# Optimization experiments

Hardware: AMD Instinct MI355X
Metric: run time of the kernel (lower is better)

## Reference

```python
import jax, jax.numpy as jnp
import numpy as np

H, W = 200, 200           # BEV spatial shape (single level)
NBQ, NH, NL, NP = 2, 8, 1, 4
D = 256
HD = D // NH


def setup_inputs() -> dict:
    key = jax.random.key(0)
    ks = jax.random.split(key, 12)
    bs, nq = 1, H * W
    query = jax.random.normal(ks[0], (bs, nq, D), jnp.float32)
    value = jax.random.normal(ks[1], (bs, NBQ * nq, D), jnp.float32)
    reference_points = jax.random.uniform(ks[2], (bs, nq, NL, 2), dtype=jnp.float32)
    spatial_shapes = jnp.array([[H, W]], dtype=jnp.int32)
    sc = 1.0 / np.sqrt(D)
    W_v = jax.random.normal(ks[3], (D, D), jnp.float32) * sc
    b_v = jax.random.normal(ks[4], (D,), jnp.float32) * 0.01
    W_so = jax.random.normal(ks[5], (2 * D, NBQ * NH * NL * NP * 2), jnp.float32) * 0.02
    b_so = jax.random.normal(ks[6], (NBQ * NH * NL * NP * 2,), jnp.float32) * 0.5
    W_aw = jax.random.normal(ks[7], (2 * D, NBQ * NH * NL * NP), jnp.float32) * 0.02
    b_aw = jax.random.normal(ks[8], (NBQ * NH * NL * NP,), jnp.float32) * 0.01
    W_o = jax.random.normal(ks[9], (D, D), jnp.float32) * sc
    b_o = jax.random.normal(ks[10], (D,), jnp.float32) * 0.01
    return {"query": query, "value": value, "reference_points": reference_points,
            "spatial_shapes": spatial_shapes,
            "W_v": W_v, "b_v": b_v, "W_so": W_so, "b_so": b_so,
            "W_aw": W_aw, "b_aw": b_aw, "W_o": W_o, "b_o": b_o}


def _ms_deform_attn(value, locs, attn):
    # value: (B, K, NH, HD); locs: (B, nq, NH, NL, NP, 2) in [0,1]; attn: (B, nq, NH, NL, NP)
    B, K, h, d = value.shape
    nq = locs.shape[1]
    out = jnp.zeros((B, nq, h, d), value.dtype)
    start = 0
    for l, (Hl, Wl) in enumerate([(H, W)]):
        v = value[:, start:start + Hl * Wl].transpose(0, 2, 1, 3).reshape(B * h, Hl * Wl, d)
        start += Hl * Wl
        g = locs[:, :, :, l]                      # (B, nq, h, NP, 2)
        # grid_sample(align_corners=False, padding='zeros') pixel coords
        x = g[..., 0] * Wl - 0.5
        y = g[..., 1] * Hl - 0.5
        x0 = jnp.floor(x); y0 = jnp.floor(y)
        lx = x - x0; ly = y - y0
        x0 = x0.astype(jnp.int32); y0 = y0.astype(jnp.int32)
        acc = jnp.zeros((B * h, nq * NP, d), value.dtype)
        for dy, wy in ((0, 1.0 - ly), (1, ly)):
            for dx, wx in ((0, 1.0 - lx), (1, lx)):
                xi = x0 + dx; yi = y0 + dy
                valid = ((xi >= 0) & (xi < Wl) & (yi >= 0) & (yi < Hl)).astype(value.dtype)
                idx = jnp.clip(yi, 0, Hl - 1) * Wl + jnp.clip(xi, 0, Wl - 1)  # (B,nq,h,NP)
                idxf = idx.transpose(0, 2, 1, 3).reshape(B * h, nq * NP)
                samp = jnp.take_along_axis(v, idxf[:, :, None], axis=1)       # (B*h, nq*NP, d)
                wgt = (wx * wy * valid).transpose(0, 2, 1, 3).reshape(B * h, nq * NP, 1)
                acc = acc + samp * wgt
        acc = acc.reshape(B, h, nq, NP, d)
        out = out + jnp.einsum('bhqpd,bqhp->bqhd', acc, attn[:, :, :, l])
    return out.reshape(B, nq, h * d)


def reference(query, value, reference_points, spatial_shapes,
              W_v, b_v, W_so, b_so, W_aw, b_aw, W_o, b_o):
    bs, nq, _ = query.shape
    identity = query
    val4 = value.reshape(bs, NBQ, nq, D)
    # query enhanced with most recent bev-queue features
    qe = jnp.concatenate([val4[:, 0], query], axis=-1)           # (bs, nq, 2D)
    vproj = (value @ W_v + b_v).reshape(bs * NBQ, nq, NH, HD)
    off = (qe @ W_so + b_so).reshape(bs, nq, NH, NBQ, NL, NP, 2)
    aw = (qe @ W_aw + b_aw).reshape(bs, nq, NH, NBQ, NL * NP)
    aw = jax.nn.softmax(aw, axis=-1).reshape(bs, nq, NH, NBQ, NL, NP)
    aw = aw.transpose(0, 3, 1, 2, 4, 5).reshape(bs * NBQ, nq, NH, NL, NP)
    # offset normalizer: [W, H] per level
    norm = jnp.stack([spatial_shapes[:, 1], spatial_shapes[:, 0]], -1).astype(query.dtype)  # (NL,2)
    locs = (reference_points[:, :, None, None, :, None, :]
            + off / norm[None, None, None, None, :, None, :])     # (bs,nq,NH,NBQ,NL,NP,2)
    locs = locs.transpose(0, 3, 1, 2, 4, 5, 6).reshape(bs * NBQ, nq, NH, NL, NP, 2)
    out = _ms_deform_attn(vproj, locs, aw)                        # (bs*NBQ, nq, D)
    out = out.reshape(bs, NBQ, nq, D).mean(axis=1)
    return out @ W_o + b_o + identity
```

## Files before the change

### kernel.cpp

```cpp
#include <hip/hip_runtime.h>
#include <math.h>

#define HW_   40000
#define NQ_   40000
#define IMGW  200
#define IMGH  200

typedef __bf16 bf16;
typedef __attribute__((ext_vector_type(4))) __bf16 bf16x4;
typedef __attribute__((ext_vector_type(8))) __bf16 bf16x8;
typedef __attribute__((ext_vector_type(4))) float f32x4;

__device__ __forceinline__ void gload_lds16(const void* g, void* l) {
  __builtin_amdgcn_global_load_lds(
      (const __attribute__((address_space(1))) void*)g,
      (__attribute__((address_space(3))) void*)l, 16, 0, 0);
}

__global__ __launch_bounds__(256) void prep_kernel(
    const float* __restrict__ Wv, const float* __restrict__ Wso,
    const float* __restrict__ Waw, const float* __restrict__ Wo,
    bf16* __restrict__ BtV, bf16* __restrict__ BtOA, bf16* __restrict__ BtO)
{
  int idx = blockIdx.x * 256 + threadIdx.x;
  if (idx < 65536) {
    int k = idx >> 8, n = idx & 255;
    BtV[(size_t)n * 256 + k] = (bf16)Wv[idx];
  } else if (idx < 131072) {
    int j = idx - 65536;
    int k = j >> 7, n = j & 127;
    BtOA[(size_t)n * 512 + k] = (bf16)Wso[j];
  } else if (idx < 163840) {
    int j = idx - 131072;
    int k = j >> 6, n = j & 63;
    BtOA[(size_t)(128 + n) * 512 + k] = (bf16)Waw[j];
  } else if (idx < 229376) {
    int j = idx - 163840;
    int k = j >> 8, n = j & 255;
    BtO[(size_t)n * 256 + k] = (bf16)Wo[j];
  }
}

template<int KT, int MODE, int BN, int ASRC>
__global__ __launch_bounds__(256) void mfma_gemm_kernel(
    const void* __restrict__ A0, const void* __restrict__ A1,
    const bf16* __restrict__ Bt,
    const float* __restrict__ bias0, const float* __restrict__ bias1,
    const float* __restrict__ resid,
    void* __restrict__ outp, void* __restrict__ outp2, int M)
{
  constexpr int NT16 = BN / 32;
  constexpr int BCH  = BN / 64;
  constexpr int NIT  = KT / 32;
  __shared__ bf16 As[2][64 * 32];
  __shared__ bf16 Bs[2][BN * 32];
  const int t    = threadIdx.x;
  const int m0   = blockIdx.x * 64;
  const int w    = t >> 6;
  const int lane = t & 63;
  const int quad = lane >> 4;
  const int l16  = lane & 15;
  const int wm   = (w & 1) * 32;
  const int wn   = (w >> 1) * (BN / 2);

  f32x4 acc[2][NT16] = {};

  int gmA;
  {
    int gm = m0 + (t >> 2);
    gmA = (gm >= M) ? (M - 1) : gm;
  }
  const int arow = t >> 2;
  const int akey = (arow >> 1) & 3;

  float4 apf[2];
  bf16x8 ah0, ah1;

  auto issueB = [&](int it) {
    const int kt  = it * 32;
    const int buf = it & 1;
#pragma unroll
    for (int i = 0; i < BCH; ++i) {
      int c   = i * 256 + t;
      int row = c >> 2;
      int j   = (c & 3) ^ ((row >> 1) & 3);
      gload_lds16(&Bt[(size_t)row * KT + kt + j * 8], &Bs[buf][c * 8]);
    }
  };

  auto issueA_lds = [&](int it) {
    const int kt  = it * 32;
    const int buf = it & 1;
    const bf16* Ap = (const bf16*)A0;
    int j = (t & 3) ^ akey;
    gload_lds16(&Ap[(size_t)gmA * 256 + kt + j * 8], &As[buf][t * 8]);
  };

  auto loadA_reg = [&](int it) {
    const int kt = it * 32;
    if (ASRC == 1) {
      const float* Ap; int col;
      if (KT == 512) { Ap = (kt < 256) ? (const float*)A0 : (const float*)A1; col = kt & 255; }
      else           { Ap = (const float*)A0; col = kt; }
      const float4* s4 = (const float4*)&Ap[(size_t)gmA * 256 + col + (t & 3) * 8];
      apf[0] = s4[0];
      apf[1] = s4[1];
    } else {
      ah0 = *(const bf16x8*)&((const bf16*)A0)[(size_t)gmA * 256 + kt + (t & 3) * 8];
      ah1 = *(const bf16x8*)&((const bf16*)A1)[(size_t)gmA * 256 + kt + (t & 3) * 8];
    }
  };

  auto writeA = [&](int it) {
    const int buf = it & 1;
    int j = (t & 3) ^ akey;
    bf16x8 o;
    if (ASRC == 1) {
      o = bf16x8{(bf16)apf[0].x, (bf16)apf[0].y, (bf16)apf[0].z, (bf16)apf[0].w,
                 (bf16)apf[1].x, (bf16)apf[1].y, (bf16)apf[1].z, (bf16)apf[1].w};
    } else {
#pragma unroll
      for (int e = 0; e < 8; ++e)
        o[e] = (bf16)(0.5f * ((float)ah0[e] + (float)ah1[e]));
    }
    *(bf16x8*)&As[buf][arow * 32 + j * 8] = o;
  };

  if (ASRC) { loadA_reg(0); issueB(0); writeA(0); }
  else      { issueA_lds(0); issueB(0); }

#pragma unroll
  for (int it = 0; it < NIT; ++it) {
    __syncthreads();
    if (it + 1 < NIT) {
      issueB(it + 1);
      if (ASRC) loadA_reg(it + 1); else issueA_lds(it + 1);
    }
    const bf16* as = As[it & 1];
    const bf16* bs = Bs[it & 1];
    bf16x8 af[2], bfr[NT16];
#pragma unroll
    for (int x = 0; x < 2; ++x) {
      int row = wm + x * 16 + l16;
      af[x] = *(const bf16x8*)&as[row * 32 + (quad ^ ((row >> 1) & 3)) * 8];
    }
#pragma unroll
    for (int x = 0; x < NT16; ++x) {
      int row = wn + x * 16 + l16;
      bfr[x] = *(const bf16x8*)&bs[row * 32 + (quad ^ ((row >> 1) & 3)) * 8];
    }
#pragma unroll
    for (int mt = 0; mt < 2; ++mt)
#pragma unroll
      for (int nt = 0; nt < NT16; ++nt)
        acc[mt][nt] = __builtin_amdgcn_mfma_f32_16x16x32_bf16(
            af[mt], bfr[nt], acc[mt][nt], 0, 0, 0);
    if (ASRC && it + 1 < NIT) writeA(it + 1);
  }

#pragma unroll
  for (int mt = 0; mt < 2; ++mt) {
#pragma unroll
    for (int r = 0; r < 4; ++r) {
      const int gm = m0 + wm + mt * 16 + quad * 4 + r;
      if (gm >= M) continue;
#pragma unroll
      for (int nt = 0; nt < NT16; ++nt) {
        const int gn = wn + nt * 16 + l16;
        float v = acc[mt][nt][r];
        if (MODE == 0) {
          int nbq = (gm >= HW_) ? 1 : 0;
          int pix = gm - nbq * HW_;
          int h = gn >> 5, hd = gn & 31;
          ((bf16*)outp)[(((size_t)(nbq * 8 + h) * HW_ + pix) << 5) + hd] =
              (bf16)(v + bias0[gn]);
        } else if (MODE == 1) {
          if (gn < 128) {
            int gg = gn >> 3, e = gn & 7;
            ((bf16*)outp)[((size_t)gg * NQ_ + gm) * 8 + e] = (bf16)(v + bias0[gn]);
          } else {
            int j = gn - 128;
            int gg = j >> 2, e = j & 3;
            ((bf16*)outp2)[((size_t)gg * NQ_ + gm) * 4 + e] = (bf16)(v + bias1[j]);
          }
        } else {
          ((float*)outp)[(size_t)gm * 256 + gn] =
              v + bias0[gn] + resid[(size_t)gm * 256 + gn];
        }
      }
    }
  }
}

__global__ __launch_bounds__(256) void deform_attn_kernel(
    const bf16* __restrict__ vws,
    const bf16* __restrict__ off_g,
    const bf16* __restrict__ aw_g,
    const float* __restrict__ ref,
    bf16* __restrict__ ms0,
    bf16* __restrict__ ms1)
{
  const int t    = threadIdx.x;
  const int w    = t >> 6;
  const int lane = t & 63;
  const int b    = blockIdx.x;
  const int nbq  = b / 5000;
  const int bb   = b - nbq * 5000;
  const int h    = bb & 7;
  const int qc   = bb >> 3;
  const int qi   = lane >> 2;
  const int sub  = lane & 3;
  const int q    = qc * 64 + w * 16 + qi;
  const int g    = h * 2 + nbq;
  bf16* msN = nbq ? ms1 : ms0;

  const float rx = ref[2 * q + 0] * (float)IMGW - 0.5f;
  const float ry = ref[2 * q + 1] * (float)IMGH - 0.5f;

  bf16x4 a4 = *(const bf16x4*)&aw_g[((size_t)g * NQ_ + q) * 4];
  float aa0 = (float)a4[0], aa1 = (float)a4[1], aa2 = (float)a4[2], aa3 = (float)a4[3];
  float mx = fmaxf(fmaxf(aa0, aa1), fmaxf(aa2, aa3));
  float e0 = __expf(aa0 - mx), e1 = __expf(aa1 - mx);
  float e2 = __expf(aa2 - mx), e3 = __expf(aa3 - mx);
  float inv = 1.0f / (e0 + e1 + e2 + e3);
  float w4[4] = {e0 * inv, e1 * inv, e2 * inv, e3 * inv};

  bf16x8 o8 = *(const bf16x8*)&off_g[((size_t)g * NQ_ + q) * 8];

  const bf16* vbase = vws + (((size_t)(nbq * 8 + h) * HW_) << 5) + sub * 8;

  float  ww[16];
  bf16x8 v[16];
#pragma unroll
  for (int p = 0; p < 4; ++p) {
    float x = rx + (float)o8[2 * p];
    float y = ry + (float)o8[2 * p + 1];
    float xf = floorf(x), yf = floorf(y);
    int   x0 = (int)xf,   y0 = (int)yf;
    float lx = x - xf,    ly = y - yf;
    int   x1 = x0 + 1,    y1 = y0 + 1;
    float w00 = (1.0f - lx) * (1.0f - ly);
    float w01 = lx * (1.0f - ly);
    float w10 = (1.0f - lx) * ly;
    float w11 = lx * ly;
    if (x0 < 0 || x0 >= IMGW) { w00 = 0.0f; w10 = 0.0f; }
    if (x1 < 0 || x1 >= IMGW) { w01 = 0.0f; w11 = 0.0f; }
    if (y0 < 0 || y0 >= IMGH) { w00 = 0.0f; w01 = 0.0f; }
    if (y1 < 0 || y1 >= IMGH) { w10 = 0.0f; w11 = 0.0f; }
    int xc0 = min(max(x0, 0), IMGW - 1), xc1 = min(max(x1, 0), IMGW - 1);
    int yc0 = min(max(y0, 0), IMGH - 1), yc1 = min(max(y1, 0), IMGH - 1);
    float wp = w4[p];
    ww[4 * p + 0] = wp * w00;
    ww[4 * p + 1] = wp * w01;
    ww[4 * p + 2] = wp * w10;
    ww[4 * p + 3] = wp * w11;
    v[4 * p + 0] = *(const bf16x8*)&vbase[(size_t)(yc0 * IMGW + xc0) << 5];
    v[4 * p + 1] = *(const bf16x8*)&vbase[(size_t)(yc0 * IMGW + xc1) << 5];
    v[4 * p + 2] = *(const bf16x8*)&vbase[(size_t)(yc1 * IMGW + xc0) << 5];
    v[4 * p + 3] = *(const bf16x8*)&vbase[(size_t)(yc1 * IMGW + xc1) << 5];
  }

  float acc[8] = {};
#pragma unroll
  for (int s = 0; s < 16; ++s)
#pragma unroll
    for (int j = 0; j < 8; ++j)
      acc[j] = fmaf(ww[s], (float)v[s][j], acc[j]);

  bf16x8 o;
#pragma unroll
  for (int j = 0; j < 8; ++j) o[j] = (bf16)acc[j];
  *(bf16x8*)&msN[(size_t)q * 256 + h * 32 + sub * 8] = o;
}

extern "C" void kernel_launch(void* const* d_in, const int* in_sizes, int n_in,
                              void* d_out, int out_size, void* d_ws, size_t ws_size,
                              hipStream_t stream) {
  const float* query = (const float*)d_in[0];
  const float* value = (const float*)d_in[1];
  const float* ref   = (const float*)d_in[2];
  const float* Wv  = (const float*)d_in[4];
  const float* bv  = (const float*)d_in[5];
  const float* Wso = (const float*)d_in[6];
  const float* bso = (const float*)d_in[7];
  const float* Waw = (const float*)d_in[8];
  const float* baw = (const float*)d_in[9];
  const float* Wo  = (const float*)d_in[10];
  const float* bo  = (const float*)d_in[11];
  float* out = (float*)d_out;

  char* p = (char*)d_ws;
  bf16* vws    = (bf16*)p; p += (size_t)2 * 8 * HW_ * 32 * 2;
  bf16* off_g  = (bf16*)p; p += (size_t)16 * NQ_ * 8 * 2;
  bf16* aw_g   = (bf16*)p; p += (size_t)16 * NQ_ * 4 * 2;
  bf16* ms0    = (bf16*)p; p += (size_t)NQ_ * 256 * 2;
  bf16* ms1    = (bf16*)p; p += (size_t)NQ_ * 256 * 2;
  bf16* BtV    = (bf16*)p; p += (size_t)256 * 256 * 2;
  bf16* BtOA   = (bf16*)p; p += (size_t)192 * 512 * 2;
  bf16* BtO    = (bf16*)p; p += (size_t)256 * 256 * 2;

  prep_kernel<<<896, 256, 0, stream>>>(Wv, Wso, Waw, Wo, BtV, BtOA, BtO);

  mfma_gemm_kernel<256, 0, 256, 1><<<1250, 256, 0, stream>>>(
      value, nullptr, BtV, bv, nullptr, nullptr, vws, nullptr, 2 * HW_);
  mfma_gemm_kernel<512, 1, 192, 1><<<625, 256, 0, stream>>>(
      value, query, BtOA, bso, baw, nullptr, off_g, aw_g, NQ_);
  deform_attn_kernel<<<10000, 256, 0, stream>>>(vws, off_g, aw_g, ref, ms0, ms1);
  mfma_gemm_kernel<256, 2, 256, 2><<<625, 256, 0, stream>>>(
      ms0, ms1, BtO, bo, nullptr, query, out, nullptr, NQ_);
}
```

Measured before the change: 296.3 us.

## Load GEMM fragments directly from global memory, dropping LDS staging

The MFMA GEMM kernel no longer stages A and B tiles through double-buffered shared memory with swizzling and barriers. Each lane now loads its own MFMA fragments straight from global memory into registers, prefetching the next A fragment while the current MFMAs run, and launch bounds now request at least two blocks per CU. This removes the __syncthreads and LDS traffic, but each wave re-reads B and A fragments that other waves share, so it leans on L1/L2 hits, and B loads are no longer prefetched ahead of use.

New measurement: 385.4 us. 1.3x slower.

```diff
diff --git a/kernel.cpp b/kernel.cpp
--- a/kernel.cpp
+++ b/kernel.cpp
@@ -10,12 +10,6 @@
 typedef __attribute__((ext_vector_type(4))) __bf16 bf16x4;
 typedef __attribute__((ext_vector_type(8))) __bf16 bf16x8;
 typedef __attribute__((ext_vector_type(4))) float f32x4;
-
-__device__ __forceinline__ void gload_lds16(const void* g, void* l) {
-  __builtin_amdgcn_global_load_lds(
-      (const __attribute__((address_space(1))) void*)g,
-      (__attribute__((address_space(3))) void*)l, 16, 0, 0);
-}
 
 __global__ __launch_bounds__(256) void prep_kernel(
     const float* __restrict__ Wv, const float* __restrict__ Wso,
@@ -42,7 +36,7 @@
 }
 
 template<int KT, int MODE, int BN, int ASRC>
-__global__ __launch_bounds__(256) void mfma_gemm_kernel(
+__global__ __launch_bounds__(256, 2) void mfma_gemm_kernel(
     const void* __restrict__ A0, const void* __restrict__ A1,
     const bf16* __restrict__ Bt,
     const float* __restrict__ bias0, const float* __restrict__ bias1,
@@ -50,10 +44,7 @@
     void* __restrict__ outp, void* __restrict__ outp2, int M)
 {
   constexpr int NT16 = BN / 32;
-  constexpr int BCH  = BN / 64;
   constexpr int NIT  = KT / 32;
-  __shared__ bf16 As[2][64 * 32];
-  __shared__ bf16 Bs[2][BN * 32];
   const int t    = threadIdx.x;
   const int m0   = blockIdx.x * 64;
   const int w    = t >> 6;
@@ -65,97 +56,75 @@
 
   f32x4 acc[2][NT16] = {};
 
-  int gmA;
-  {
-    int gm = m0 + (t >> 2);
-    gmA = (gm >= M) ? (M - 1) : gm;
-  }
-  const int arow = t >> 2;
-  const int akey = (arow >> 1) & 3;
-
-  float4 apf[2];
-  bf16x8 ah0, ah1;
-
-  auto issueB = [&](int it) {
-    const int kt  = it * 32;
-    const int buf = it & 1;
-#pragma unroll
-    for (int i = 0; i < BCH; ++i) {
-      int c   = i * 256 + t;
-      int row = c >> 2;
-      int j   = (c & 3) ^ ((row >> 1) & 3);
-      gload_lds16(&Bt[(size_t)row * KT + kt + j * 8], &Bs[buf][c * 8]);
-    }
-  };
-
-  auto issueA_lds = [&](int it) {
-    const int kt  = it * 32;
-    const int buf = it & 1;
-    const bf16* Ap = (const bf16*)A0;
-    int j = (t & 3) ^ akey;
-    gload_lds16(&Ap[(size_t)gmA * 256 + kt + j * 8], &As[buf][t * 8]);
-  };
-
-  auto loadA_reg = [&](int it) {
+  int aoff[2];
+#pragma unroll
+  for (int x = 0; x < 2; ++x) {
+    int r = m0 + wm + x * 16 + l16;
+    if (r >= M) r = M - 1;
+    aoff[x] = r * 256 + quad * 8;
+  }
+  int boff[NT16];
+#pragma unroll
+  for (int x = 0; x < NT16; ++x)
+    boff[x] = (wn + x * 16 + l16) * KT + quad * 8;
+
+  float4 apf[2][2];
+  bf16x8 ah[2][2];
+
+  auto loadA = [&](int it) {
     const int kt = it * 32;
     if (ASRC == 1) {
       const float* Ap; int col;
       if (KT == 512) { Ap = (kt < 256) ? (const float*)A0 : (const float*)A1; col = kt & 255; }
       else           { Ap = (const float*)A0; col = kt; }
-      const float4* s4 = (const float4*)&Ap[(size_t)gmA * 256 + col + (t & 3) * 8];
-      apf[0] = s4[0];
-      apf[1] = s4[1];
+#pragma unroll
+      for (int x = 0; x < 2; ++x) {
+        const float4* s = (const float4*)&Ap[(size_t)(aoff[x] + col)];
+        apf[x][0] = s[0];
+        apf[x][1] = s[1];
+      }
     } else {
-      ah0 = *(const bf16x8*)&((const bf16*)A0)[(size_t)gmA * 256 + kt + (t & 3) * 8];
-      ah1 = *(const bf16x8*)&((const bf16*)A1)[(size_t)gmA * 256 + kt + (t & 3) * 8];
+#pragma unroll
+      for (int x = 0; x < 2; ++x) {
+        ah[x][0] = *(const bf16x8*)&((const bf16*)A0)[(size_t)aoff[x] + kt];
+        ah[x][1] = *(const bf16x8*)&((const bf16*)A1)[(size_t)aoff[x] + kt];
+      }
     }
   };
 
-  auto writeA = [&](int it) {
-    const int buf = it & 1;
-    int j = (t & 3) ^ akey;
-    bf16x8 o;
+  loadA(0);
+
+#pragma unroll
+  for (int it = 0; it < NIT; ++it) {
+    const int kt = it * 32;
+    bf16x8 br[NT16];
+#pragma unroll
+    for (int x = 0; x < NT16; ++x)
+      br[x] = *(const bf16x8*)&Bt[(size_t)boff[x] + kt];
+
+    bf16x8 af[2];
     if (ASRC == 1) {
-      o = bf16x8{(bf16)apf[0].x, (bf16)apf[0].y, (bf16)apf[0].z, (bf16)apf[0].w,
-                 (bf16)apf[1].x, (bf16)apf[1].y, (bf16)apf[1].z, (bf16)apf[1].w};
+#pragma unroll
+      for (int x = 0; x < 2; ++x) {
+        float4 lo = apf[x][0], hi = apf[x][1];
+        af[x] = bf16x8{(bf16)lo.x, (bf16)lo.y, (bf16)lo.z, (bf16)lo.w,
+                       (bf16)hi.x, (bf16)hi.y, (bf16)hi.z, (bf16)hi.w};
+      }
     } else {
 #pragma unroll
-      for (int e = 0; e < 8; ++e)
-        o[e] = (bf16)(0.5f * ((float)ah0[e] + (float)ah1[e]));
+      for (int x = 0; x < 2; ++x)
+#pragma unroll
+        for (int e = 0; e < 8; ++e)
+          af[x][e] = (bf16)(0.5f * ((float)ah[x][0][e] + (float)ah[x][1][e]));
     }
-    *(bf16x8*)&As[buf][arow * 32 + j * 8] = o;
-  };
-
-  if (ASRC) { loadA_reg(0); issueB(0); writeA(0); }
-  else      { issueA_lds(0); issueB(0); }
-
-#pragma unroll
-  for (int it = 0; it < NIT; ++it) {
-    __syncthreads();
-    if (it + 1 < NIT) {
-      issueB(it + 1);
-      if (ASRC) loadA_reg(it + 1); else issueA_lds(it + 1);
-    }
-    const bf16* as = As[it & 1];
-    const bf16* bs = Bs[it & 1];
-    bf16x8 af[2], bfr[NT16];
-#pragma unroll
-    for (int x = 0; x < 2; ++x) {
-      int row = wm + x * 16 + l16;
-      af[x] = *(const bf16x8*)&as[row * 32 + (quad ^ ((row >> 1) & 3)) * 8];
-    }
-#pragma unroll
-    for (int x = 0; x < NT16; ++x) {
-      int row = wn + x * 16 + l16;
-      bfr[x] = *(const bf16x8*)&bs[row * 32 + (quad ^ ((row >> 1) & 3)) * 8];
-    }
+    if (it + 1 < NIT) loadA(it + 1);
+
 #pragma unroll
     for (int mt = 0; mt < 2; ++mt)
 #pragma unroll
       for (int nt = 0; nt < NT16; ++nt)
         acc[mt][nt] = __builtin_amdgcn_mfma_f32_16x16x32_bf16(
-            af[mt], bfr[nt], acc[mt][nt], 0, 0, 0);
-    if (ASRC && it + 1 < NIT) writeA(it + 1);
+            af[mt], br[nt], acc[mt][nt], 0, 0, 0);
   }
 
 #pragma unroll
```
